# Performance work log

Hardware: AMD Instinct MI355X
Metric: run time of the kernel (lower is better)

## Reference

```python
import jax, jax.numpy as jnp
import numpy as np
from jax import lax

NUM_SEGMENTS = 50
HIDDEN = 128
IN_CH = 64
LOGSIG_DIM = IN_CH + IN_CH * (IN_CH - 1) // 2 + IN_CH  # level1 + Levy area + startpoint


def setup_inputs() -> dict:
    key = jax.random.key(0)
    k0, k1, k2, k3, k4 = jax.random.split(key, 5)
    B, C, T, V = 16, IN_CH, 200, 25
    x = jax.random.normal(k0, (B, C, T, V), dtype=jnp.float32)
    s = 1.0 / np.sqrt(HIDDEN).astype(np.float32)
    W_ih = jax.random.uniform(k1, (4 * HIDDEN, LOGSIG_DIM), jnp.float32, -s, s)
    W_hh = jax.random.uniform(k2, (4 * HIDDEN, HIDDEN), jnp.float32, -s, s)
    b_ih = jax.random.uniform(k3, (4 * HIDDEN,), jnp.float32, -s, s)
    b_hh = jax.random.uniform(k4, (4 * HIDDEN,), jnp.float32, -s, s)
    return {"x": x, "W_ih": W_ih, "W_hh": W_hh, "b_ih": b_ih, "b_hh": b_hh}


def _segment_logsig(xn):
    # xn: (N, C, T). Split T into NUM_SEGMENTS chunks; level-2 log-signature per chunk.
    N, C, T = xn.shape
    L = T // NUM_SEGMENTS  # points per segment
    p = xn.transpose(0, 2, 1).reshape(N, NUM_SEGMENTS, L, C)  # path points
    start = p[:, :, 0]                                  # (N,S,C) segment startpoint
    inc = p[:, :, 1:] - p[:, :, :-1]                    # (N,S,L-1,C) increments
    dev = p[:, :, :-1] - start[:, :, None]              # (N,S,L-1,C) p_t - p_0
    # Level-2 iterated integrals (cross terms): S2_ij = sum_t dev_t,i * inc_t,j
    S2 = jnp.einsum('nsti,nstj->nsij', dev, inc)        # (N,S,C,C)
    A = 0.5 * (S2 - S2.transpose(0, 1, 3, 2))           # Levy area (antisymmetric part)
    iu, ju = jnp.triu_indices(C, k=1)
    levy = A[:, :, iu, ju]                              # (N,S,C(C-1)/2)
    lvl1 = p[:, :, -1] - start                          # (N,S,C) level-1 term
    return jnp.concatenate([lvl1, levy, start], axis=-1)  # (N,S,LOGSIG_DIM)


def _lstm(seq, W_ih, W_hh, b_ih, b_hh):
    # seq: (N, S, F). Single-layer unidirectional LSTM, torch gate order (i,f,g,o).
    N = seq.shape[0]
    x_proj = jnp.einsum('nsf,gf->nsg', seq, W_ih) + b_ih + b_hh  # (N,S,4H)

    def step(carry, xt):
        h, c = carry
        gates = xt + h @ W_hh.T
        i, f, g, o = jnp.split(gates, 4, axis=-1)
        c = jax.nn.sigmoid(f) * c + jax.nn.sigmoid(i) * jnp.tanh(g)
        h = jax.nn.sigmoid(o) * jnp.tanh(c)
        return (h, c), h

    h0 = jnp.zeros((N, HIDDEN), seq.dtype)
    c0 = jnp.zeros((N, HIDDEN), seq.dtype)
    _, hs = lax.scan(step, (h0, c0), x_proj.transpose(1, 0, 2))
    return hs.transpose(1, 0, 2)  # (N,S,H)


def reference(x, W_ih, W_hh, b_ih, b_hh):
    B, C, T, V = x.shape
    xn = x.transpose(0, 3, 1, 2).reshape(B * V, C, T)
    ls = _segment_logsig(xn)                      # (B*V, S, LOGSIG_DIM)
    h = _lstm(ls, W_ih, W_hh, b_ih, b_hh)          # (B*V, S, H)
    out = h.reshape(B, V, NUM_SEGMENTS, HIDDEN).transpose(0, 3, 2, 1)
    return out  # (B, H, S, V)
```

## Files before the change

### kernel.cpp

```cpp
#include <hip/hip_runtime.h>
#include <stdint.h>

#define NSEG 50
#define HID 128
#define KDIM 2144
#define KD2 2176
#define KD2B 4352
#define NROW 20000
#define NROW_PAD 20096
#define GATES 512
#define NSEQ 400

typedef __attribute__((ext_vector_type(8))) _Float16 f16x8;
typedef __attribute__((ext_vector_type(4))) float f32x4;
typedef __attribute__((ext_vector_type(4))) uint32_t u32x4;

#define GLB_SPACE __attribute__((address_space(1)))
#define LDS_SPACE __attribute__((address_space(3)))

__device__ __forceinline__ void g2lds16(const void* g, void* l) {
    __builtin_amdgcn_global_load_lds((const GLB_SPACE uint32_t*)g,
                                     (LDS_SPACE uint32_t*)l, 16, 0, 0);
}

__global__ __launch_bounds__(256) void prep_kernel(const float* __restrict__ Wih,
                                                   const float* __restrict__ Whh,
                                                   const float* __restrict__ bih,
                                                   const float* __restrict__ bhh,
                                                   _Float16* __restrict__ wh,
                                                   _Float16* __restrict__ whh16,
                                                   float* __restrict__ bias) {
    int idx = blockIdx.x * 256 + threadIdx.x;
    const int nwih = 512 * KD2;
    const int nwhh = 512 * HID;
    if (idx < nwih) {
        int row = idx / KD2;
        int k = idx - row * KD2;
        wh[idx] = (k < KDIM) ? (_Float16)Wih[row * KDIM + k] : (_Float16)0.0f;
    } else if (idx < nwih + nwhh) {
        int q = idx - nwih;
        whh16[q] = (_Float16)Whh[q];
    } else if (idx < nwih + nwhh + 512) {
        int g = idx - nwih - nwhh;
        bias[g] = bih[g] + bhh[g];
    }
}

__global__ __launch_bounds__(256) void feat_kernel(const float* __restrict__ x,
                                                   _Float16* __restrict__ feat) {
    int bid = blockIdx.x;
    int b = bid / NSEG;
    int s = bid - b * NSEG;
    int tid = threadIdx.x;

    __shared__ float pbuf[64 * 100];
    __shared__ float2 uu[25 * 64];
    __shared__ float2 vvb[25 * 64];

    for (int i = tid; i < 6400; i += 256) {
        int c = i / 100;
        int r = i - c * 100;
        pbuf[c * 100 + r] = x[(((size_t)b * 64 + c) * 200 + 4 * s) * 25 + r];
    }
    if (tid < 800) {
        int v = tid >> 5;
        int k = 2144 + (tid & 31);
        size_t m = ((size_t)(b * 25 + v)) * NSEG + s;
        feat[m * KD2 + k] = (_Float16)0.0f;
    }
    __syncthreads();

    for (int i = tid; i < 1600; i += 256) {
        int v = i >> 6;
        int c = i & 63;
        float p0 = pbuf[c * 100 + v];
        float p1 = pbuf[c * 100 + 25 + v];
        float p2 = pbuf[c * 100 + 50 + v];
        float p3 = pbuf[c * 100 + 75 + v];
        uu[v * 64 + c] = make_float2(p1 - p0, p2 - p0);
        vvb[v * 64 + c] = make_float2(p2 - p1, p3 - p2);
        size_t m = ((size_t)(b * 25 + v)) * NSEG + s;
        feat[m * KD2 + c] = (_Float16)(p3 - p0);
        feat[m * KD2 + 2080 + c] = (_Float16)p0;
    }
    __syncthreads();

    for (int ch = 0; ch < 8; ch++) {
        int pidx = ch * 256 + tid;
        if (pidx < 2016) {
            float disc = 16129.0f - 8.0f * (float)pidx;
            int i = (int)((127.0f - sqrtf(disc)) * 0.5f);
            int off = 63 * i - (i * (i - 1)) / 2;
            while (off > pidx) { i--; off = 63 * i - (i * (i - 1)) / 2; }
            while (63 * (i + 1) - ((i + 1) * i) / 2 <= pidx) { i++; off = 63 * i - (i * (i - 1)) / 2; }
            int j = pidx - off + i + 1;
            int k = 64 + pidx;
            for (int v = 0; v < 25; v++) {
                float2 ui = uu[v * 64 + i], uj = uu[v * 64 + j];
                float2 vi = vvb[v * 64 + i], vj = vvb[v * 64 + j];
                float val = 0.5f * (ui.x * vj.x - uj.x * vi.x + ui.y * vj.y - uj.y * vi.y);
                size_t m = ((size_t)(b * 25 + v)) * NSEG + s;
                feat[m * KD2 + k] = (_Float16)val;
            }
        }
    }
}

__global__ __launch_bounds__(256, 3) void gemm_kernel(const _Float16* __restrict__ feat,
                                                      const _Float16* __restrict__ wh,
                                                      const float* __restrict__ bias,
                                                      _Float16* __restrict__ xproj2) {
    int bid = blockIdx.x;
    int x = bid & 7;
    int t = bid >> 3;
    int nb = t & 3;
    int mt = (t >> 2) * 8 + x;
    if (mt >= 157) return;
    int m0 = mt * 128;
    int n0 = nb * 128;
    int tid = threadIdx.x;
    int wave = tid >> 6;
    int lane = tid & 63;
    int quad = lane >> 4;
    int l15 = lane & 15;
    int wm = (wave & 1) * 64;
    int wn = (wave >> 1) * 64;

    int r8 = lane >> 3;
    int gcol = ((lane & 7) * 16) ^ (r8 * 16);

    __shared__ __align__(16) _Float16 smem[16896];
    char* As = (char*)smem;
    char* Bs = (char*)smem + 128 * 128;

    const f32x4 z4 = {0.f, 0.f, 0.f, 0.f};
    f32x4 acc[4][4];
    for (int i = 0; i < 4; i++)
        for (int j = 0; j < 4; j++) acc[i][j] = z4;

    const char* featB = (const char*)feat;
    const char* whB = (const char*)wh;

    for (int kt = 0; kt < 34; kt++) {
        size_t kb = (size_t)kt * 128;
        __syncthreads();
        for (int it = 0; it < 4; it++) {
            int rb = it * 32 + wave * 8;
            g2lds16(featB + (size_t)(m0 + rb + r8) * KD2B + kb + gcol, As + rb * 128);
            g2lds16(whB + (size_t)(n0 + rb + r8) * KD2B + kb + gcol, Bs + rb * 128);
        }
        __syncthreads();

        for (int ks = 0; ks < 2; ks++) {
            int off = ((ks * 64) | (quad * 16)) ^ ((l15 & 7) * 16);
            f16x8 af[4], bf[4];
            for (int tt = 0; tt < 4; tt++) {
                af[tt] = *(const f16x8*)(As + (wm + tt * 16 + l15) * 128 + off);
                bf[tt] = *(const f16x8*)(Bs + (wn + tt * 16 + l15) * 128 + off);
            }
            for (int mtl = 0; mtl < 4; mtl++)
                for (int ntl = 0; ntl < 4; ntl++)
                    acc[mtl][ntl] = __builtin_amdgcn_mfma_f32_16x16x32_f16(af[mtl], bf[ntl], acc[mtl][ntl], 0, 0, 0);
        }
    }

    __syncthreads();
    for (int ntl = 0; ntl < 4; ntl++) {
        int nl = wn + ntl * 16 + l15;
        float bv = bias[n0 + nl];
        for (int mtl = 0; mtl < 4; mtl++)
            for (int r = 0; r < 4; r++) {
                int ml = wm + mtl * 16 + quad * 4 + r;
                smem[ml * 132 + nl] = (_Float16)(acc[mtl][ntl][r] + bv);
            }
    }
    __syncthreads();
    {
        int row = tid >> 1;
        int seg = tid & 1;
        int m = m0 + row;
        if (m < NROW) {
            unsigned q = (unsigned)m / 50u;
            unsigned s = (unsigned)m - q * 50u;
            const char* src = (const char*)smem + row * 264 + seg * 128;
            char* dst = (char*)xproj2 + ((size_t)s * NSEQ + q) * 1024 + (size_t)n0 * 2 + seg * 128;
            for (int i = 0; i < 8; i++)
                *(u32x4*)(dst + i * 16) = *(const u32x4*)(src + i * 16);
        }
    }
}

__global__ __launch_bounds__(512, 2) void lstm_kernel(const _Float16* __restrict__ xproj2,
                                                      const _Float16* __restrict__ whh,
                                                      _Float16* __restrict__ hseq) {
    int bid = blockIdx.x;
    int tid = threadIdx.x;
    int wave = tid >> 6;
    int lane = tid & 63;
    int quad = lane >> 4;
    int col = lane & 15;
    int hid = wave * 16 + col;

    __shared__ __align__(16) char xbuf[2 * 4 * 1040];
    __shared__ __align__(16) _Float16 hbuf[2][4 * 136];

    f16x8 bfrag[4][4];
    for (int g = 0; g < 4; g++) {
        int n = g * 128 + hid;
        for (int kq = 0; kq < 4; kq++)
            bfrag[g][kq] = *(const f16x8*)(whh + (size_t)n * HID + kq * 32 + quad * 8);
    }
    for (int i = tid; i < 2 * 4 * 136; i += 512) ((_Float16*)hbuf)[i] = (_Float16)0.0f;
    float cst = 0.0f;
    _Float16 hprev = (_Float16)0.0f;

    const char* xsrc = (const char*)xproj2;
    if (wave < 4)
        g2lds16(xsrc + (size_t)(bid * 4 + wave) * 1024 + lane * 16, xbuf + wave * 1040);
    __syncthreads();

    const f32x4 z4 = {0.f, 0.f, 0.f, 0.f};
    for (int s = 0; s < NSEG; s++) {
        int cur = s & 1;
        int nxt = cur ^ 1;

        if (s > 0)
            hseq[((size_t)(s - 1) * NSEQ + bid * 4 + quad) * HID + hid] = hprev;
        if (s + 1 < NSEG && wave < 4)
            g2lds16(xsrc + ((size_t)(s + 1) * NSEQ + bid * 4 + wave) * 1024 + lane * 16,
                    xbuf + nxt * 4160 + wave * 1040);

        f16x8 afrag[4];
        for (int kq = 0; kq < 4; kq++)
            afrag[kq] = *(const f16x8*)(&hbuf[cur][(col & 3) * 136 + kq * 32 + quad * 8]);

        float xp[4];
        for (int g = 0; g < 4; g++)
            xp[g] = (float)(*(const _Float16*)(xbuf + cur * 4160 +
                           quad * 1040 + (g * 128 + hid) * 2));

        f32x4 acc[4];
        for (int g = 0; g < 4; g++) {
            acc[g] = z4;
            for (int kq = 0; kq < 4; kq++)
                acc[g] = __builtin_amdgcn_mfma_f32_16x16x32_f16(afrag[kq], bfrag[g][kq], acc[g], 0, 0, 0);
        }

        float gv[4];
        for (int g = 0; g < 4; g++) {
            float lo = (quad & 1) ? acc[g][1] : acc[g][0];
            float hi = (quad & 1) ? acc[g][3] : acc[g][2];
            gv[g] = (quad & 2) ? hi : lo;
        }

        float ip = gv[0] + xp[0];
        float fp = gv[1] + xp[1];
        float gp = gv[2] + xp[2];
        float op = gv[3] + xp[3];
        float si = __fdividef(1.0f, 1.0f + __expf(-ip));
        float sf = __fdividef(1.0f, 1.0f + __expf(-fp));
        float so = __fdividef(1.0f, 1.0f + __expf(-op));
        float eg = __expf(-2.0f * gp);
        float tg = __fdividef(1.0f - eg, 1.0f + eg);
        cst = sf * cst + si * tg;
        float ec = __expf(-2.0f * cst);
        float tc = __fdividef(1.0f - ec, 1.0f + ec);
        float hv = so * tc;
        hprev = (_Float16)hv;
        hbuf[nxt][quad * 136 + hid] = hprev;
        __syncthreads();
    }
    hseq[((size_t)(NSEG - 1) * NSEQ + bid * 4 + quad) * HID + hid] = hprev;
}

__global__ __launch_bounds__(256) void tr_kernel(const _Float16* __restrict__ hseq,
                                                 float* __restrict__ out) {
    int bid = blockIdx.x;
    int b = bid / NSEG;
    int s = bid - b * NSEG;
    int tid = threadIdx.x;

    __shared__ _Float16 buf[25 * 130];

    const uint32_t* src32 = (const uint32_t*)(hseq + ((size_t)s * NSEQ + b * 25) * HID);
    uint32_t* buf32 = (uint32_t*)buf;
    for (int i = tid; i < 1600; i += 256) {
        int v = i >> 6;
        int d = i & 63;
        buf32[v * 65 + d] = src32[i];
    }
    __syncthreads();
    for (int i = tid; i < 3200; i += 256) {
        int hid = i / 25;
        int v = i - hid * 25;
        out[(((size_t)b * 128 + hid) * NSEG + s) * 25 + v] = (float)buf[v * 130 + hid];
    }
}

extern "C" void kernel_launch(void* const* d_in, const int* in_sizes, int n_in,
                              void* d_out, int out_size, void* d_ws, size_t ws_size,
                              hipStream_t stream) {
    const float* x = (const float*)d_in[0];
    const float* Wih = (const float*)d_in[1];
    const float* Whh = (const float*)d_in[2];
    const float* bih = (const float*)d_in[3];
    const float* bhh = (const float*)d_in[4];
    float* out = (float*)d_out;

    char* ws = (char*)d_ws;
    size_t off = 0;
    _Float16* feat = (_Float16*)(ws + off);   off += (size_t)NROW_PAD * KD2 * 2;
    _Float16* xproj2 = (_Float16*)(ws + off); off += (size_t)NSEG * NSEQ * GATES * 2;
    _Float16* hseq = (_Float16*)(ws + off);   off += (size_t)NSEG * NSEQ * HID * 2;
    _Float16* wh = (_Float16*)(ws + off);     off += (size_t)512 * KD2 * 2;
    _Float16* whh16 = (_Float16*)(ws + off);  off += (size_t)512 * HID * 2;
    float* bias = (float*)(ws + off);         off += 512 * 4;

    int prep_total = 512 * KD2 + 512 * HID + 512;
    hipLaunchKernelGGL(prep_kernel, dim3((prep_total + 255) / 256), dim3(256), 0, stream,
                       Wih, Whh, bih, bhh, wh, whh16, bias);
    hipLaunchKernelGGL(feat_kernel, dim3(16 * NSEG), dim3(256), 0, stream, x, feat);
    hipLaunchKernelGGL(gemm_kernel, dim3(640), dim3(256), 0, stream, feat, wh, bias, xproj2);
    hipLaunchKernelGGL(lstm_kernel, dim3(100), dim3(512), 0, stream, xproj2, whh16, hseq);
    hipLaunchKernelGGL(tr_kernel, dim3(16 * NSEG), dim3(256), 0, stream, hseq, out);
}
```

Baseline: 225.5 us.

## Bulk-stage LSTM inputs in LDS and buffer hidden states for coalesced writeout

The LSTM kernel now loads half of its sequence's input projections (25 steps) into LDS in one bulk transfer, rather than prefetching one step per iteration. Hidden states are kept in an LDS history buffer and written to global memory in one coalesced pass at the end, instead of a scattered store every step. This takes global memory latency and store waits out of the serial recurrence. It costs about 157KB of LDS, which limits each CU to one block, and adds a synchronous reload between the two halves. The feature kernel also packs its two float2 LDS arrays into one float4 array to save LDS reads.

```diff
diff --git a/kernel.cpp b/kernel.cpp
--- a/kernel.cpp
+++ b/kernel.cpp
@@ -54,8 +54,7 @@
     int tid = threadIdx.x;
 
     __shared__ float pbuf[64 * 100];
-    __shared__ float2 uu[25 * 64];
-    __shared__ float2 vvb[25 * 64];
+    __shared__ __align__(16) float4 uv4[25 * 64];
 
     for (int i = tid; i < 6400; i += 256) {
         int c = i / 100;
@@ -77,8 +76,7 @@
         float p1 = pbuf[c * 100 + 25 + v];
         float p2 = pbuf[c * 100 + 50 + v];
         float p3 = pbuf[c * 100 + 75 + v];
-        uu[v * 64 + c] = make_float2(p1 - p0, p2 - p0);
-        vvb[v * 64 + c] = make_float2(p2 - p1, p3 - p2);
+        uv4[v * 64 + c] = make_float4(p1 - p0, p2 - p0, p2 - p1, p3 - p2);
         size_t m = ((size_t)(b * 25 + v)) * NSEG + s;
         feat[m * KD2 + c] = (_Float16)(p3 - p0);
         feat[m * KD2 + 2080 + c] = (_Float16)p0;
@@ -96,9 +94,9 @@
             int j = pidx - off + i + 1;
             int k = 64 + pidx;
             for (int v = 0; v < 25; v++) {
-                float2 ui = uu[v * 64 + i], uj = uu[v * 64 + j];
-                float2 vi = vvb[v * 64 + i], vj = vvb[v * 64 + j];
-                float val = 0.5f * (ui.x * vj.x - uj.x * vi.x + ui.y * vj.y - uj.y * vi.y);
+                float4 a = uv4[v * 64 + i];
+                float4 bb = uv4[v * 64 + j];
+                float val = 0.5f * (a.x * bb.z - bb.x * a.z + a.y * bb.w - bb.y * a.w);
                 size_t m = ((size_t)(b * 25 + v)) * NSEG + s;
                 feat[m * KD2 + k] = (_Float16)val;
             }
@@ -201,8 +199,9 @@
     int col = lane & 15;
     int hid = wave * 16 + col;
 
-    __shared__ __align__(16) char xbuf[2 * 4 * 1040];
-    __shared__ __align__(16) _Float16 hbuf[2][4 * 136];
+    __shared__ __align__(16) char xbuf[25 * 4 * 1040];
+    __shared__ __align__(16) _Float16 hst[NSEG * 4 * HID];
+    __shared__ __align__(16) _Float16 hbuf[2][4 * 144];
 
     f16x8 bfrag[4][4];
     for (int g = 0; g < 4; g++) {
@@ -210,67 +209,80 @@
         for (int kq = 0; kq < 4; kq++)
             bfrag[g][kq] = *(const f16x8*)(whh + (size_t)n * HID + kq * 32 + quad * 8);
     }
-    for (int i = tid; i < 2 * 4 * 136; i += 512) ((_Float16*)hbuf)[i] = (_Float16)0.0f;
+    for (int i = tid; i < 2 * 4 * 144; i += 512) ((_Float16*)hbuf)[i] = (_Float16)0.0f;
     float cst = 0.0f;
-    _Float16 hprev = (_Float16)0.0f;
 
     const char* xsrc = (const char*)xproj2;
-    if (wave < 4)
-        g2lds16(xsrc + (size_t)(bid * 4 + wave) * 1024 + lane * 16, xbuf + wave * 1040);
+    for (int r = wave; r < 100; r += 8)
+        g2lds16(xsrc + ((size_t)((r >> 2) * NSEQ + bid * 4 + (r & 3))) * 1024 + lane * 16,
+                xbuf + r * 1040);
     __syncthreads();
 
     const f32x4 z4 = {0.f, 0.f, 0.f, 0.f};
-    for (int s = 0; s < NSEG; s++) {
-        int cur = s & 1;
-        int nxt = cur ^ 1;
-
-        if (s > 0)
-            hseq[((size_t)(s - 1) * NSEQ + bid * 4 + quad) * HID + hid] = hprev;
-        if (s + 1 < NSEG && wave < 4)
-            g2lds16(xsrc + ((size_t)(s + 1) * NSEQ + bid * 4 + wave) * 1024 + lane * 16,
-                    xbuf + nxt * 4160 + wave * 1040);
-
-        f16x8 afrag[4];
-        for (int kq = 0; kq < 4; kq++)
-            afrag[kq] = *(const f16x8*)(&hbuf[cur][(col & 3) * 136 + kq * 32 + quad * 8]);
-
-        float xp[4];
-        for (int g = 0; g < 4; g++)
-            xp[g] = (float)(*(const _Float16*)(xbuf + cur * 4160 +
-                           quad * 1040 + (g * 128 + hid) * 2));
-
-        f32x4 acc[4];
-        for (int g = 0; g < 4; g++) {
-            acc[g] = z4;
+    for (int half = 0; half < 2; half++) {
+        for (int ss = 0; ss < 25; ss++) {
+            int s = half * 25 + ss;
+            int cur = s & 1;
+            int nxt = cur ^ 1;
+
+            f16x8 afrag[4];
             for (int kq = 0; kq < 4; kq++)
-                acc[g] = __builtin_amdgcn_mfma_f32_16x16x32_f16(afrag[kq], bfrag[g][kq], acc[g], 0, 0, 0);
-        }
-
-        float gv[4];
-        for (int g = 0; g < 4; g++) {
-            float lo = (quad & 1) ? acc[g][1] : acc[g][0];
-            float hi = (quad & 1) ? acc[g][3] : acc[g][2];
-            gv[g] = (quad & 2) ? hi : lo;
-        }
-
-        float ip = gv[0] + xp[0];
-        float fp = gv[1] + xp[1];
-        float gp = gv[2] + xp[2];
-        float op = gv[3] + xp[3];
-        float si = __fdividef(1.0f, 1.0f + __expf(-ip));
-        float sf = __fdividef(1.0f, 1.0f + __expf(-fp));
-        float so = __fdividef(1.0f, 1.0f + __expf(-op));
-        float eg = __expf(-2.0f * gp);
-        float tg = __fdividef(1.0f - eg, 1.0f + eg);
-        cst = sf * cst + si * tg;
-        float ec = __expf(-2.0f * cst);
-        float tc = __fdividef(1.0f - ec, 1.0f + ec);
-        float hv = so * tc;
-        hprev = (_Float16)hv;
-        hbuf[nxt][quad * 136 + hid] = hprev;
-        __syncthreads();
-    }
-    hseq[((size_t)(NSEG - 1) * NSEQ + bid * 4 + quad) * HID + hid] = hprev;
+                afrag[kq] = *(const f16x8*)(&hbuf[cur][(col & 3) * 144 + kq * 32 + quad * 8]);
+
+            float xp[4];
+            for (int g = 0; g < 4; g++)
+                xp[g] = (float)(*(const _Float16*)(xbuf + (ss * 4 + quad) * 1040 +
+                               (g * 128 + hid) * 2));
+
+            f32x4 acc[4];
+            for (int g = 0; g < 4; g++) {
+                acc[g] = z4;
+                for (int kq = 0; kq < 4; kq++)
+                    acc[g] = __builtin_amdgcn_mfma_f32_16x16x32_f16(afrag[kq], bfrag[g][kq], acc[g], 0, 0, 0);
+            }
+
+            float gv[4];
+            for (int g = 0; g < 4; g++) {
+                float lo = (quad & 1) ? acc[g][1] : acc[g][0];
+                float hi = (quad & 1) ? acc[g][3] : acc[g][2];
+                gv[g] = (quad & 2) ? hi : lo;
+            }
+
+            float ip = gv[0] + xp[0];
+            float fp = gv[1] + xp[1];
+            float gp = gv[2] + xp[2];
+            float op = gv[3] + xp[3];
+            float si = __fdividef(1.0f, 1.0f + __expf(-ip));
+            float sf = __fdividef(1.0f, 1.0f + __expf(-fp));
+            float so = __fdividef(1.0f, 1.0f + __expf(-op));
+            float eg = __expf(-2.0f * gp);
+            float tg = __fdividef(1.0f - eg, 1.0f + eg);
+            cst = sf * cst + si * tg;
+            float ec = __expf(-2.0f * cst);
+            float tc = __fdividef(1.0f - ec, 1.0f + ec);
+            float hv = so * tc;
+            _Float16 hv16 = (_Float16)hv;
+            hbuf[nxt][quad * 144 + hid] = hv16;
+            hst[(s * 4 + quad) * 128 + hid] = hv16;
+            __syncthreads();
+        }
+        if (half == 0) {
+            for (int r = wave; r < 100; r += 8)
+                g2lds16(xsrc + ((size_t)((25 + (r >> 2)) * NSEQ + bid * 4 + (r & 3))) * 1024 + lane * 16,
+                        xbuf + r * 1040);
+            __syncthreads();
+        }
+    }
+
+    const u32x4* src = (const u32x4*)hst;
+    for (int i = tid; i < 3200; i += 512) {
+        int s = i >> 6;
+        int rem = i & 63;
+        int seq = rem >> 4;
+        int seg = rem & 15;
+        u32x4 v = src[i];
+        *(u32x4*)((char*)hseq + ((size_t)(s * NSEQ + bid * 4 + seq)) * 256 + seg * 16) = v;
+    }
 }
 
 __global__ __launch_bounds__(256) void tr_kernel(const _Float16* __restrict__ hseq,
```

Measured after the change: 220.5 us. -2.2%, faster.
